# Performance work log

Measured on AMD Instinct MI355X. Metric: run time of the kernel, lower is better.

Reference implementation:

```python
import jax, jax.numpy as jnp
import numpy as np

BINS = 256
MAXV = float(2 ** 14 - 1)
LAP_K = jnp.array([[0.0, 1.0, 0.0], [1.0, -4.0, 1.0], [0.0, 1.0, 0.0]], jnp.float32).reshape(1, 1, 3, 3)


def _soft_hist_entropy(flat):
    # flat: (B, N) in arbitrary range; per-image min-max normalize to [0,1]
    fmin = jnp.min(flat, axis=1, keepdims=True)
    fmax = jnp.max(flat, axis=1, keepdims=True)
    rng = fmax - fmin
    rng = jnp.where(rng == 0, jnp.ones_like(rng), rng)
    x = jnp.clip((flat - fmin) / rng, 0.0, 1.0)
    # Triangular soft-histogram weights clamp(1-|x-c_k|/bw, 0) are nonzero for at
    # most the 2 bins adjacent to x, so scatter-add instead of a (B,N,BINS) tensor.
    p = x * BINS - 0.5            # position in bin-center coordinates
    i0 = jnp.floor(p)
    w1 = p - i0                   # weight on bin i0+1
    w0 = 1.0 - w1                 # weight on bin i0
    i0i = i0.astype(jnp.int32)
    i1i = i0i + 1
    v0 = (i0i >= 0) & (i0i < BINS)
    v1 = (i1i >= 0) & (i1i < BINS)

    def hist_one(idx0, idx1, a0, a1, m0, m1):
        h = jnp.zeros((BINS,), flat.dtype)
        h = h.at[jnp.clip(idx0, 0, BINS - 1)].add(jnp.where(m0, a0, 0.0))
        h = h.at[jnp.clip(idx1, 0, BINS - 1)].add(jnp.where(m1, a1, 0.0))
        return h

    hist = jax.vmap(hist_one)(i0i, i1i, w0, w1, v0, v1)  # (B, BINS)
    hist = hist / (jnp.sum(hist, axis=1, keepdims=True) + 1e-10)
    ent = -jnp.sum(hist * jnp.log2(hist + 1e-10), axis=1)
    return ent / jnp.float32(np.log2(BINS))


def _extract_features(image):
    # normalize 14-bit input to [0,1] iff values exceed 1 (matches torch branch)
    image = jnp.where(jnp.max(image) > 1.0, image / MAXV, image)
    B = image.shape[0]
    flat = image.reshape(B, -1)
    variance = jnp.var(flat, axis=1, ddof=1)   # torch.var is unbiased
    mn = jnp.min(flat, axis=1)
    mx = jnp.max(flat, axis=1)
    ent = _soft_hist_entropy(flat)
    lap = jax.lax.conv_general_dilated(
        image, LAP_K, window_strides=(1, 1), padding=[(1, 1), (1, 1)],
        dimension_numbers=('NCHW', 'OIHW', 'NCHW'))
    lap_var = jnp.var(lap.reshape(B, -1), axis=1, ddof=1)
    return jnp.stack([variance, mn, mx, ent, lap_var], axis=1)  # (B, 5)


def setup_inputs() -> dict:
    key = jax.random.key(0)
    ks = jax.random.split(key, 4)
    image = jax.random.uniform(ks[0], (16, 1, 1024, 1280), jnp.float32) * MAXV
    # Kaiming normal fan_in (relu): std = sqrt(2 / fan_in); biases zero
    W1 = jax.random.normal(ks[1], (64, 5), jnp.float32) * np.float32(np.sqrt(2.0 / 5))
    W2 = jax.random.normal(ks[2], (64, 64), jnp.float32) * np.float32(np.sqrt(2.0 / 64))
    W3 = jax.random.normal(ks[3], (3, 64), jnp.float32) * np.float32(np.sqrt(2.0 / 64))
    return {
        'image': image,
        'W1': W1, 'b1': jnp.zeros((64,), jnp.float32),
        'W2': W2, 'b2': jnp.zeros((64,), jnp.float32),
        'W3': W3, 'b3': jnp.zeros((3,), jnp.float32),
    }


def reference(image, W1, b1, W2, b2, W3, b3):
    feats = _extract_features(image)                       # (B, 5)
    h = jax.nn.relu(feats @ W1.T + b1)
    h = jax.nn.relu(h @ W2.T + b2)
    logits = h @ W3.T + b3                                  # (B, 3)
    probs = jax.nn.softmax(logits, axis=1)
    class_ids = jnp.argmax(probs, axis=1)
    return class_ids, probs, feats
```

## Files before the change

### kernel.cpp

```cpp
#include <hip/hip_runtime.h>
#include <cfloat>
#include <math.h>

#define IMG_B 16
#define IMG_H 1024
#define IMG_W 1280
#define NPIX (IMG_H * IMG_W)
#define BINS 256
#define SLICES 64
#define NBLK (IMG_B * SLICES)
#define F4_PER_SLICE (16 * IMG_W / 4)

__device__ __forceinline__ unsigned encf(float f) {
    unsigned u = __float_as_uint(f);
    return (u >> 31) ? ~u : (u | 0x80000000u);
}
__device__ __forceinline__ float decf(unsigned u) {
    unsigned b = (u & 0x80000000u) ? (u & 0x7fffffffu) : ~u;
    return __uint_as_float(b);
}


__global__ __launch_bounds__(256) void k_pre(const float* __restrict__ img,
                                             uint2* __restrict__ mmp,
                                             double* __restrict__ mom) {
    const int blk = blockIdx.x;
    const int tid = threadIdx.x;
    const int b   = blk >> 6;
    const int sl  = blk & 63;
    const int lane = tid & 63, wv = tid >> 6;

    const float* base = img + (size_t)b * NPIX;
    const int r0 = sl * 16;

    float fs = 0.f, fs2 = 0.f, fls = 0.f, fls2 = 0.f;
    float fmn = FLT_MAX, fmx = -FLT_MAX;

    #pragma unroll 2
    for (int k = 0; k < 20; ++k) {
        int i   = tid + k * 256;
        int ri  = i / 320;
        int c   = i - ri * 320;
        int r   = r0 + ri;
        const float* rowf = base + (size_t)r * IMG_W;
        float4 m = ((const float4*)rowf)[c];
        float4 up = make_float4(0.f, 0.f, 0.f, 0.f);
        float4 dn = make_float4(0.f, 0.f, 0.f, 0.f);
        if (r > 0)          up = ((const float4*)(rowf - IMG_W))[c];
        if (r < IMG_H - 1)  dn = ((const float4*)(rowf + IMG_W))[c];
        float lft = (c > 0)   ? rowf[4 * c - 1] : 0.f;
        float rgt = (c < 319) ? rowf[4 * c + 4] : 0.f;

        fs  += (m.x + m.y) + (m.z + m.w);
        fs2 += (m.x * m.x + m.y * m.y) + (m.z * m.z + m.w * m.w);
        fmn = fminf(fmn, fminf(fminf(m.x, m.y), fminf(m.z, m.w)));
        fmx = fmaxf(fmx, fmaxf(fmaxf(m.x, m.y), fmaxf(m.z, m.w)));

        float l0 = up.x + dn.x + lft + m.y - 4.f * m.x;
        float l1 = up.y + dn.y + m.x + m.z - 4.f * m.y;
        float l2 = up.z + dn.z + m.y + m.w - 4.f * m.z;
        float l3 = up.w + dn.w + m.z + rgt - 4.f * m.w;
        fls  += (l0 + l1) + (l2 + l3);
        fls2 += (l0 * l0 + l1 * l1) + (l2 * l2 + l3 * l3);
    }

    for (int o = 32; o; o >>= 1) {
        fs   += __shfl_down(fs,   (unsigned)o, 64);
        fs2  += __shfl_down(fs2,  (unsigned)o, 64);
        fls  += __shfl_down(fls,  (unsigned)o, 64);
        fls2 += __shfl_down(fls2, (unsigned)o, 64);
        fmn = fminf(fmn, __shfl_down(fmn, (unsigned)o, 64));
        fmx = fmaxf(fmx, __shfl_down(fmx, (unsigned)o, 64));
    }
    __shared__ float swred[4][4];
    __shared__ float rmn[4], rmx[4];
    if (lane == 0) {
        swred[0][wv] = fs;  swred[1][wv] = fs2;
        swred[2][wv] = fls; swred[3][wv] = fls2;
        rmn[wv] = fmn; rmx[wv] = fmx;
    }
    __syncthreads();
    if (tid == 0) {
        double S   = (double)swred[0][0] + (double)swred[0][1] + (double)swred[0][2] + (double)swred[0][3];
        double S2  = (double)swred[1][0] + (double)swred[1][1] + (double)swred[1][2] + (double)swred[1][3];
        double LS  = (double)swred[2][0] + (double)swred[2][1] + (double)swred[2][2] + (double)swred[2][3];
        double LS2 = (double)swred[3][0] + (double)swred[3][1] + (double)swred[3][2] + (double)swred[3][3];
        mom[blk * 4 + 0] = S;  mom[blk * 4 + 1] = S2;
        mom[blk * 4 + 2] = LS; mom[blk * 4 + 3] = LS2;
        float mn = fminf(fminf(rmn[0], rmn[1]), fminf(rmn[2], rmn[3]));
        float mx = fmaxf(fmaxf(rmx[0], rmx[1]), fmaxf(rmx[2], rmx[3]));
        mmp[blk] = make_uint2(encf(mn), encf(mx));
    }
}

__global__ __launch_bounds__(256) void k_hist(const float* __restrict__ img,
                                              const uint2* __restrict__ mmp,
                                              unsigned* __restrict__ bhist) {
    const int blk = blockIdx.x;
    const int tid = threadIdx.x;
    const int b   = blk >> 6;

    __shared__ unsigned long long lh64[BINS + 1];
    __shared__ float sh_ab[2];

    if (tid < 64) {
        uint2 e = mmp[b * 64 + tid];
        unsigned emn = e.x, emx = e.y;
        for (int o = 32; o; o >>= 1) {
            emn = min(emn, (unsigned)__shfl_down(emn, (unsigned)o, 64));
            emx = max(emx, (unsigned)__shfl_down(emx, (unsigned)o, 64));
        }
        if (tid == 0) {
            float fmn = decf(emn), fmx = decf(emx);
            float rng = fmx - fmn;
            if (rng == 0.f) rng = 1.f;
            float a = 256.f / rng;
            float bb = -fmn * a - 0.5f;
            sh_ab[0] = a; sh_ab[1] = bb;
        }
    }
    lh64[tid] = 0ull;
    if (tid == 0) lh64[BINS] = 0ull;
    __syncthreads();

    const float a = sh_ab[0], bb = sh_ab[1];

    const float4* p = (const float4*)img + (size_t)blk * F4_PER_SLICE;
    #pragma unroll 2
    for (int k = 0; k < 20; ++k) {
        float4 v = p[tid + k * 256];
        #pragma unroll
        for (int j = 0; j < 4; ++j) {
            float vv = (j == 0) ? v.x : (j == 1) ? v.y : (j == 2) ? v.z : v.w;
            float pp = fminf(fmaxf(vv * a + bb, -0.5f), 255.5f);
            float fi = floorf(pp);
            int   i0 = (int)fi;
            unsigned w1q = (unsigned)((pp - fi) * 65536.f + 0.5f);
            atomicAdd(&lh64[i0 + 1], 0x100000000ull + (unsigned long long)w1q);
        }
    }
    __syncthreads();

    unsigned long long a0 = lh64[tid];
    unsigned long long a1 = lh64[tid + 1];
    unsigned long long h  = ((a1 >> 32) << 16) - (a1 & 0xffffffffull) + (a0 & 0xffffffffull);
    bhist[blk * BINS + tid] = (unsigned)h;
}

__global__ __launch_bounds__(256) void k_final(
    const unsigned* __restrict__ bhist, const double* __restrict__ mom,
    const uint2* __restrict__ mmp,
    const float* __restrict__ W1, const float* __restrict__ b1,
    const float* __restrict__ W2, const float* __restrict__ b2,
    const float* __restrict__ W3, const float* __restrict__ b3,
    float* __restrict__ out)
{
    const int ib = blockIdx.x;
    const int tid = threadIdx.x;
    const int lane = tid & 63, wv = tid >> 6;

    __shared__ double dred[4];
    __shared__ float  fred[4];
    __shared__ double smom[4];
    __shared__ unsigned smm2[2];
    __shared__ unsigned sgm[4];
    __shared__ float f5[5], h1[64], h2[64], lg[3];

    double h = 0.0;
    for (int s = 0; s < 64; ++s)
        h += (double)bhist[(ib * 64 + s) * BINS + tid];

    double tot = h;
    for (int o = 32; o; o >>= 1) tot += __shfl_down(tot, (unsigned)o, 64);
    if (lane == 0) dred[wv] = tot;
    __syncthreads();
    tot = dred[0] + dred[1] + dred[2] + dred[3];

    double hv = h * (1.0 / 65536.0);
    double tv = tot * (1.0 / 65536.0);
    float hn = (float)(hv / (tv + 1e-10));
    float ce = hn * log2f(hn + 1e-10f);
    for (int o = 32; o; o >>= 1) ce += __shfl_down(ce, (unsigned)o, 64);
    if (lane == 0) fred[wv] = ce;

    if (tid < 64) {
        double q0 = mom[(ib * 64 + tid) * 4 + 0];
        double q1 = mom[(ib * 64 + tid) * 4 + 1];
        double q2 = mom[(ib * 64 + tid) * 4 + 2];
        double q3 = mom[(ib * 64 + tid) * 4 + 3];
        uint2 e = mmp[ib * 64 + tid];
        unsigned emn = e.x, emx = e.y;
        for (int o = 32; o; o >>= 1) {
            q0 += __shfl_down(q0, (unsigned)o, 64);
            q1 += __shfl_down(q1, (unsigned)o, 64);
            q2 += __shfl_down(q2, (unsigned)o, 64);
            q3 += __shfl_down(q3, (unsigned)o, 64);
            emn = min(emn, (unsigned)__shfl_down(emn, (unsigned)o, 64));
            emx = max(emx, (unsigned)__shfl_down(emx, (unsigned)o, 64));
        }
        if (tid == 0) {
            smom[0] = q0; smom[1] = q1; smom[2] = q2; smom[3] = q3;
            smm2[0] = emn; smm2[1] = emx;
        }
    }
    {
        unsigned g = max(max(mmp[tid].y, mmp[256 + tid].y),
                         max(mmp[512 + tid].y, mmp[768 + tid].y));
        for (int o = 32; o; o >>= 1)
            g = max(g, (unsigned)__shfl_down(g, (unsigned)o, 64));
        if (lane == 0) sgm[wv] = g;
    }
    __syncthreads();

    if (tid == 0) {
        float ent = -(fred[0] + fred[1] + fred[2] + fred[3]) / 8.f;
        float gmax = decf(max(max(sgm[0], sgm[1]), max(sgm[2], sgm[3])));
        float sc = (gmax > 1.f) ? (1.f / 16383.f) : 1.f;
        double N = (double)NPIX;
        double S = smom[0], S2 = smom[1], LS = smom[2], LS2 = smom[3];
        double sc2 = (double)sc * (double)sc;
        float var  = (float)((S2  - S  * S  / N) / (N - 1.0) * sc2);
        float lvar = (float)((LS2 - LS * LS / N) / (N - 1.0) * sc2);
        float mn = decf(smm2[0]) * sc;
        float mx = decf(smm2[1]) * sc;
        float* fo = out + 64 + ib * 5;
        fo[0] = var; fo[1] = mn; fo[2] = mx; fo[3] = ent; fo[4] = lvar;
        f5[0] = var; f5[1] = mn; f5[2] = mx; f5[3] = ent; f5[4] = lvar;
    }
    __syncthreads();

    if (tid < 64) {
        float aa = b1[tid];
        #pragma unroll
        for (int k = 0; k < 5; ++k) aa += W1[tid * 5 + k] * f5[k];
        h1[tid] = fmaxf(aa, 0.f);
    }
    __syncthreads();
    if (tid < 64) {
        float a2 = b2[tid];
        #pragma unroll
        for (int k = 0; k < 64; ++k) a2 += W2[tid * 64 + k] * h1[k];
        h2[tid] = fmaxf(a2, 0.f);
    }
    __syncthreads();
    if (tid < 3) {
        float a3 = b3[tid];
        #pragma unroll
        for (int k = 0; k < 64; ++k) a3 += W3[tid * 64 + k] * h2[k];
        lg[tid] = a3;
    }
    __syncthreads();
    if (tid == 0) {
        float m = fmaxf(lg[0], fmaxf(lg[1], lg[2]));
        float e0 = expf(lg[0] - m), e1 = expf(lg[1] - m), e2 = expf(lg[2] - m);
        float inv = 1.f / (e0 + e1 + e2);
        float p0 = e0 * inv, p1 = e1 * inv, p2 = e2 * inv;
        out[16 + ib * 3 + 0] = p0;
        out[16 + ib * 3 + 1] = p1;
        out[16 + ib * 3 + 2] = p2;
        int cid = 0; float bm = p0;
        if (p1 > bm) { bm = p1; cid = 1; }
        if (p2 > bm) { bm = p2; cid = 2; }
        out[ib] = (float)cid;
    }
}

extern "C" void kernel_launch(void* const* d_in, const int* in_sizes, int n_in,
                              void* d_out, int out_size, void* d_ws, size_t ws_size,
                              hipStream_t stream) {
    const float* img = (const float*)d_in[0];
    const float* W1  = (const float*)d_in[1];
    const float* b1  = (const float*)d_in[2];
    const float* W2  = (const float*)d_in[3];
    const float* b2  = (const float*)d_in[4];
    const float* W3  = (const float*)d_in[5];
    const float* b3  = (const float*)d_in[6];
    float* out = (float*)d_out;

    char* ws = (char*)d_ws;
    uint2*    mmp   = (uint2*)ws;
    double*   mom   = (double*)(ws + 8192);
    unsigned* bhist = (unsigned*)(ws + 40960);

    k_pre  <<<NBLK, 256, 0, stream>>>(img, mmp, mom);
    k_hist <<<NBLK, 256, 0, stream>>>(img, mmp, bhist);
    k_final<<<IMG_B, 256, 0, stream>>>(bhist, mom, mmp,
                                       W1, b1, W2, b2, W3, b3, out);
}
```

Before: 158.1 us.

## Enlarge pre-pass slices, shuffle neighbor pixels, and privatize histograms per wave

The pre-pass now gives each block 32 rows instead of 16, halving the block count, so fewer halo rows are reloaded. Left and right Laplacian neighbors now come from wave shuffles instead of extra scalar global loads, with a load kept only at wave edges. The histogram kernel gives each wavefront its own shared-memory histogram to cut atomic contention, and merges the four copies at the end. The downstream reductions are adjusted for 32 partials per image. The trade-off is less parallelism in the pre-pass and four times the LDS for the histogram.

```diff
diff --git a/kernel.cpp b/kernel.cpp
--- a/kernel.cpp
+++ b/kernel.cpp
@@ -7,9 +7,14 @@
 #define IMG_W 1280
 #define NPIX (IMG_H * IMG_W)
 #define BINS 256
-#define SLICES 64
-#define NBLK (IMG_B * SLICES)
-#define F4_PER_SLICE (16 * IMG_W / 4)
+
+#define PRE_SLICES 32
+#define PRE_NBLK (IMG_B * PRE_SLICES)
+#define PRE_ITERS 40
+
+#define H_SLICES 64
+#define H_NBLK (IMG_B * H_SLICES)
+#define F4_PER_HSLICE (16 * IMG_W / 4)
 
 __device__ __forceinline__ unsigned encf(float f) {
     unsigned u = __float_as_uint(f);
@@ -26,18 +31,18 @@
                                              double* __restrict__ mom) {
     const int blk = blockIdx.x;
     const int tid = threadIdx.x;
-    const int b   = blk >> 6;
-    const int sl  = blk & 63;
+    const int b   = blk >> 5;
+    const int sl  = blk & 31;
     const int lane = tid & 63, wv = tid >> 6;
 
     const float* base = img + (size_t)b * NPIX;
-    const int r0 = sl * 16;
+    const int r0 = sl * 32;
 
     float fs = 0.f, fs2 = 0.f, fls = 0.f, fls2 = 0.f;
     float fmn = FLT_MAX, fmx = -FLT_MAX;
 
     #pragma unroll 2
-    for (int k = 0; k < 20; ++k) {
+    for (int k = 0; k < PRE_ITERS; ++k) {
         int i   = tid + k * 256;
         int ri  = i / 320;
         int c   = i - ri * 320;
@@ -48,8 +53,11 @@
         float4 dn = make_float4(0.f, 0.f, 0.f, 0.f);
         if (r > 0)          up = ((const float4*)(rowf - IMG_W))[c];
         if (r < IMG_H - 1)  dn = ((const float4*)(rowf + IMG_W))[c];
-        float lft = (c > 0)   ? rowf[4 * c - 1] : 0.f;
-        float rgt = (c < 319) ? rowf[4 * c + 4] : 0.f;
+
+        float lft = __shfl_up(m.w, 1u, 64);
+        if (lane == 0)  lft = (c > 0)   ? rowf[4 * c - 1] : 0.f;
+        float rgt = __shfl_down(m.x, 1u, 64);
+        if (lane == 63) rgt = (c < 319) ? rowf[4 * c + 4] : 0.f;
 
         fs  += (m.x + m.y) + (m.z + m.w);
         fs2 += (m.x * m.x + m.y * m.y) + (m.z * m.z + m.w * m.w);
@@ -99,14 +107,15 @@
     const int blk = blockIdx.x;
     const int tid = threadIdx.x;
     const int b   = blk >> 6;
-
-    __shared__ unsigned long long lh64[BINS + 1];
+    const int wv  = tid >> 6;
+
+    __shared__ unsigned long long lh64[4][BINS + 1];
     __shared__ float sh_ab[2];
 
-    if (tid < 64) {
-        uint2 e = mmp[b * 64 + tid];
+    if (tid < 32) {
+        uint2 e = mmp[b * 32 + tid];
         unsigned emn = e.x, emx = e.y;
-        for (int o = 32; o; o >>= 1) {
+        for (int o = 16; o; o >>= 1) {
             emn = min(emn, (unsigned)__shfl_down(emn, (unsigned)o, 64));
             emx = max(emx, (unsigned)__shfl_down(emx, (unsigned)o, 64));
         }
@@ -119,13 +128,14 @@
             sh_ab[0] = a; sh_ab[1] = bb;
         }
     }
-    lh64[tid] = 0ull;
-    if (tid == 0) lh64[BINS] = 0ull;
+    for (int i = tid; i < 4 * (BINS + 1); i += 256)
+        ((unsigned long long*)lh64)[i] = 0ull;
     __syncthreads();
 
     const float a = sh_ab[0], bb = sh_ab[1];
-
-    const float4* p = (const float4*)img + (size_t)blk * F4_PER_SLICE;
+    unsigned long long* mylh = lh64[wv];
+
+    const float4* p = (const float4*)img + (size_t)blk * F4_PER_HSLICE;
     #pragma unroll 2
     for (int k = 0; k < 20; ++k) {
         float4 v = p[tid + k * 256];
@@ -136,13 +146,13 @@
             float fi = floorf(pp);
             int   i0 = (int)fi;
             unsigned w1q = (unsigned)((pp - fi) * 65536.f + 0.5f);
-            atomicAdd(&lh64[i0 + 1], 0x100000000ull + (unsigned long long)w1q);
-        }
-    }
-    __syncthreads();
-
-    unsigned long long a0 = lh64[tid];
-    unsigned long long a1 = lh64[tid + 1];
+            atomicAdd(&mylh[i0 + 1], 0x100000000ull + (unsigned long long)w1q);
+        }
+    }
+    __syncthreads();
+
+    unsigned long long a0 = lh64[0][tid]     + lh64[1][tid]     + lh64[2][tid]     + lh64[3][tid];
+    unsigned long long a1 = lh64[0][tid + 1] + lh64[1][tid + 1] + lh64[2][tid + 1] + lh64[3][tid + 1];
     unsigned long long h  = ((a1 >> 32) << 16) - (a1 & 0xffffffffull) + (a0 & 0xffffffffull);
     bhist[blk * BINS + tid] = (unsigned)h;
 }
@@ -183,14 +193,14 @@
     for (int o = 32; o; o >>= 1) ce += __shfl_down(ce, (unsigned)o, 64);
     if (lane == 0) fred[wv] = ce;
 
-    if (tid < 64) {
-        double q0 = mom[(ib * 64 + tid) * 4 + 0];
-        double q1 = mom[(ib * 64 + tid) * 4 + 1];
-        double q2 = mom[(ib * 64 + tid) * 4 + 2];
-        double q3 = mom[(ib * 64 + tid) * 4 + 3];
-        uint2 e = mmp[ib * 64 + tid];
+    if (tid < 32) {
+        double q0 = mom[(ib * 32 + tid) * 4 + 0];
+        double q1 = mom[(ib * 32 + tid) * 4 + 1];
+        double q2 = mom[(ib * 32 + tid) * 4 + 2];
+        double q3 = mom[(ib * 32 + tid) * 4 + 3];
+        uint2 e = mmp[ib * 32 + tid];
         unsigned emn = e.x, emx = e.y;
-        for (int o = 32; o; o >>= 1) {
+        for (int o = 16; o; o >>= 1) {
             q0 += __shfl_down(q0, (unsigned)o, 64);
             q1 += __shfl_down(q1, (unsigned)o, 64);
             q2 += __shfl_down(q2, (unsigned)o, 64);
@@ -204,8 +214,7 @@
         }
     }
     {
-        unsigned g = max(max(mmp[tid].y, mmp[256 + tid].y),
-                         max(mmp[512 + tid].y, mmp[768 + tid].y));
+        unsigned g = max(mmp[tid].y, mmp[256 + tid].y);
         for (int o = 32; o; o >>= 1)
             g = max(g, (unsigned)__shfl_down(g, (unsigned)o, 64));
         if (lane == 0) sgm[wv] = g;
@@ -279,11 +288,11 @@
 
     char* ws = (char*)d_ws;
     uint2*    mmp   = (uint2*)ws;
-    double*   mom   = (double*)(ws + 8192);
-    unsigned* bhist = (unsigned*)(ws + 40960);
-
-    k_pre  <<<NBLK, 256, 0, stream>>>(img, mmp, mom);
-    k_hist <<<NBLK, 256, 0, stream>>>(img, mmp, bhist);
-    k_final<<<IMG_B, 256, 0, stream>>>(bhist, mom, mmp,
-                                       W1, b1, W2, b2, W3, b3, out);
-}
+    double*   mom   = (double*)(ws + 4096);
+    unsigned* bhist = (unsigned*)(ws + 20480);
+
+    k_pre  <<<PRE_NBLK, 256, 0, stream>>>(img, mmp, mom);
+    k_hist <<<H_NBLK,   256, 0, stream>>>(img, mmp, bhist);
+    k_final<<<IMG_B,    256, 0, stream>>>(bhist, mom, mmp,
+                                          W1, b1, W2, b2, W3, b3, out);
+}
```

Result: slower. 171.3 us (+8.3%).
